# Kernel optimization log

Measured on AMD Instinct MI355X. Metric: run time of the kernel, lower is better.

## Reference

```python
import jax, jax.numpy as jnp
import numpy as np

EPS = 1e-5

def layernorm(x, g, b):
    xf = x.astype(jnp.float32)
    mu = jnp.mean(xf, axis=-1, keepdims=True)
    var = jnp.mean(jnp.square(xf - mu), axis=-1, keepdims=True)
    return ((xf - mu) * jax.lax.rsqrt(var + EPS) * g + b).astype(x.dtype)

def setup_inputs() -> dict:
    key = jax.random.key(0)
    ks = jax.random.split(key, 8)
    B, L, D_NODE, D_PAIR = 2, 512, 256, 128
    single = jax.random.normal(ks[0], (B, L, D_NODE), dtype=jnp.float32)
    pair = jax.random.normal(ks[1], (B, L, L, D_PAIR), dtype=jnp.float32)
    s = 1.0 / np.sqrt(D_NODE)
    Wa = jax.random.normal(ks[2], (D_PAIR, D_NODE), dtype=jnp.float32) * s
    ba = jnp.zeros((D_PAIR,), jnp.float32)
    Wb = jax.random.normal(ks[3], (D_PAIR, D_NODE), dtype=jnp.float32) * s
    bb = jnp.zeros((D_PAIR,), jnp.float32)
    # out layer is init='final' (zeros) in the original; use small random weights
    # so the reference output is non-trivial (same math).
    Wo = jax.random.normal(ks[4], (D_PAIR, D_PAIR), dtype=jnp.float32) * (1.0 / np.sqrt(D_PAIR))
    bo = jnp.zeros((D_PAIR,), jnp.float32)
    norm_g = jnp.ones((D_NODE,), jnp.float32)
    norm_b = jnp.zeros((D_NODE,), jnp.float32)
    pnorm_g = jnp.ones((D_PAIR,), jnp.float32)
    pnorm_b = jnp.zeros((D_PAIR,), jnp.float32)
    return dict(single=single, pair=pair, norm_g=norm_g, norm_b=norm_b,
                Wa=Wa, ba=ba, Wb=Wb, bb=bb, Wo=Wo, bo=bo,
                pnorm_g=pnorm_g, pnorm_b=pnorm_b)

def reference(single, pair, norm_g, norm_b, Wa, ba, Wb, bb, Wo, bo, pnorm_g, pnorm_b):
    x = layernorm(single, norm_g, norm_b)          # (B, L, D_NODE)
    a = x @ Wa.T + ba                               # (B, L, D_PAIR)
    b = x @ Wb.T + bb                               # (B, L, D_PAIR)
    outer = jnp.einsum('bid,bjd->bijd', a, b)       # (B, L, L, D_PAIR)
    upd = outer @ Wo.T + bo                         # (B, L, L, D_PAIR)
    return layernorm(pair + upd, pnorm_g, pnorm_b)
```

## Files before the change

### kernel.cpp

```cpp
#include <hip/hip_runtime.h>

#define BB   2
#define LL   512
#define DN   256
#define DP   128
#define TJ   64
#define LDSW 136

using bf16x8 = __attribute__((ext_vector_type(8))) short;
using f32x4  = __attribute__((ext_vector_type(4))) float;

__device__ inline unsigned short f2bf(float f) {
    unsigned int u = __float_as_uint(f);
    u += 0x7FFFu + ((u >> 16) & 1u);
    return (unsigned short)(u >> 16);
}

__global__ __launch_bounds__(256) void pu_ln_ab(
    const float* __restrict__ single, const float* __restrict__ norm_g,
    const float* __restrict__ norm_b, const float* __restrict__ Wa,
    const float* __restrict__ ba, const float* __restrict__ Wb,
    const float* __restrict__ bbias, float* __restrict__ abuf,
    unsigned short* __restrict__ bbuf)
{
    __shared__ __attribute__((aligned(16))) float xs[DN];
    __shared__ float red[8];
    const int row = blockIdx.x;
    const int tid = threadIdx.x;

    float v = single[row * DN + tid];
    float s1 = v, s2 = v * v;
    #pragma unroll
    for (int m = 32; m; m >>= 1) {
        s1 += __shfl_xor(s1, m);
        s2 += __shfl_xor(s2, m);
    }
    const int w = tid >> 6;
    if ((tid & 63) == 0) { red[w] = s1; red[4 + w] = s2; }
    __syncthreads();
    s1 = red[0] + red[1] + red[2] + red[3];
    s2 = red[4] + red[5] + red[6] + red[7];
    const float mu  = s1 * (1.0f / DN);
    const float var = s2 * (1.0f / DN) - mu * mu;
    const float rs  = rsqrtf(var + 1e-5f);
    xs[tid] = (v - mu) * rs * norm_g[tid] + norm_b[tid];
    __syncthreads();

    const int half = tid >> 7, p = tid & 127;
    const float4* W4 = (const float4*)((half ? Wb : Wa) + p * DN);
    const float4* x4 = (const float4*)xs;
    float acc = 0.f;
    #pragma unroll 8
    for (int d = 0; d < DN / 4; d++) {
        float4 wv = W4[d], xv = x4[d];
        acc += wv.x * xv.x + wv.y * xv.y + wv.z * xv.z + wv.w * xv.w;
    }
    acc += (half ? bbias[p] : ba[p]);
    if (half == 0) abuf[row * DP + p] = acc;
    else           bbuf[row * DP + p] = f2bf(acc);
}

__global__ __launch_bounds__(256) void pu_outer_ln(
    const float* __restrict__ pr, const float* __restrict__ Wo,
    const float* __restrict__ bo, const float* __restrict__ png,
    const float* __restrict__ pnb, const float* __restrict__ abuf,
    const unsigned short* __restrict__ bbuf, float* __restrict__ out)
{
    __shared__ __attribute__((aligned(16))) unsigned short sW[DP * LDSW];
    __shared__ __attribute__((aligned(16))) unsigned short sB[TJ * LDSW];

    const int jt  = blockIdx.x;
    const int i   = blockIdx.y;
    const int bz  = blockIdx.z;
    const int tid = threadIdx.x;
    const int j0  = jt * TJ;

    const int lane = tid & 63;
    const int w    = tid >> 6;
    const int m    = lane & 15;
    const int q    = lane >> 4;

    const size_t obase = (((size_t)bz * LL + i) * LL + (j0 + w * 16)) * DP;
    float pv[4][8];
    #pragma unroll
    for (int r = 0; r < 4; r++) {
        const size_t rowoff = obase + (size_t)(q * 4 + r) * DP + m;
        #pragma unroll
        for (int t = 0; t < 8; t++) pv[r][t] = pr[rowoff + t * 16];
    }

    float bo_r[8], g_r[8], pb_r[8];
    #pragma unroll
    for (int t = 0; t < 8; t++) {
        bo_r[t] = bo[t * 16 + m];
        g_r[t]  = png[t * 16 + m];
        pb_r[t] = pnb[t * 16 + m];
    }

    const float* arow = abuf + ((size_t)bz * LL + i) * DP;
    #pragma unroll
    for (int e = 0; e < 8; e++) {
        const int v  = tid + e * 256;
        const int pw = v >> 4;
        const int d0 = (v & 15) * 8;
        const float4* w4 = (const float4*)(Wo + pw * DP + d0);
        const float4* a4 = (const float4*)(arow + d0);
        float4 wa = w4[0], wb = w4[1], aa = a4[0], ab = a4[1];
        uint4 pk;
        pk.x = (unsigned)f2bf(wa.x * aa.x) | ((unsigned)f2bf(wa.y * aa.y) << 16);
        pk.y = (unsigned)f2bf(wa.z * aa.z) | ((unsigned)f2bf(wa.w * aa.w) << 16);
        pk.z = (unsigned)f2bf(wb.x * ab.x) | ((unsigned)f2bf(wb.y * ab.y) << 16);
        pk.w = (unsigned)f2bf(wb.z * ab.z) | ((unsigned)f2bf(wb.w * ab.w) << 16);
        *(uint4*)&sW[pw * LDSW + d0] = pk;
    }

    const uint4* bsrc = (const uint4*)(bbuf + ((size_t)bz * LL + j0) * DP);
    #pragma unroll
    for (int e = 0; e < 4; e++) {
        const int v  = tid + e * 256;
        const int jr = v >> 4;
        const int d0 = (v & 15) * 8;
        *(uint4*)&sB[jr * LDSW + d0] = bsrc[v];
    }
    __syncthreads();

    f32x4 acc[8];
    #pragma unroll
    for (int t = 0; t < 8; t++) { f32x4 z = {0.f, 0.f, 0.f, 0.f}; acc[t] = z; }

    const unsigned short* Abase = sB + (w * 16 + m) * LDSW + q * 8;
    const unsigned short* Bbase = sW + m * LDSW + q * 8;
    #pragma unroll
    for (int s = 0; s < 4; s++) {
        bf16x8 af = *(const bf16x8*)(Abase + s * 32);
        #pragma unroll
        for (int t = 0; t < 8; t++) {
            bf16x8 bf = *(const bf16x8*)(Bbase + t * 16 * LDSW + s * 32);
            acc[t] = __builtin_amdgcn_mfma_f32_16x16x32_bf16(af, bf, acc[t], 0, 0, 0);
        }
    }

    #pragma unroll
    for (int r = 0; r < 4; r++) {
        const size_t rowoff = obase + (size_t)(q * 4 + r) * DP + m;
        float v[8], s1 = 0.f, s2 = 0.f;
        #pragma unroll
        for (int t = 0; t < 8; t++) {
            v[t] = pv[r][t] + acc[t][r] + bo_r[t];
            s1 += v[t];
            s2 += v[t] * v[t];
        }
        s1 += __shfl_xor(s1, 1); s2 += __shfl_xor(s2, 1);
        s1 += __shfl_xor(s1, 2); s2 += __shfl_xor(s2, 2);
        s1 += __shfl_xor(s1, 4); s2 += __shfl_xor(s2, 4);
        s1 += __shfl_xor(s1, 8); s2 += __shfl_xor(s2, 8);
        const float mu  = s1 * (1.0f / DP);
        const float var = s2 * (1.0f / DP) - mu * mu;
        const float rs  = rsqrtf(var + 1e-5f);
        #pragma unroll
        for (int t = 0; t < 8; t++)
            out[rowoff + t * 16] = (v[t] - mu) * rs * g_r[t] + pb_r[t];
    }
}

extern "C" void kernel_launch(void* const* d_in, const int* in_sizes, int n_in,
                              void* d_out, int out_size, void* d_ws, size_t ws_size,
                              hipStream_t stream) {
    const float* single = (const float*)d_in[0];
    const float* pair   = (const float*)d_in[1];
    const float* norm_g = (const float*)d_in[2];
    const float* norm_b = (const float*)d_in[3];
    const float* Wa     = (const float*)d_in[4];
    const float* ba     = (const float*)d_in[5];
    const float* Wb     = (const float*)d_in[6];
    const float* bb     = (const float*)d_in[7];
    const float* Wo     = (const float*)d_in[8];
    const float* bo     = (const float*)d_in[9];
    const float* png    = (const float*)d_in[10];
    const float* pnb    = (const float*)d_in[11];
    float* out = (float*)d_out;

    float* abuf = (float*)d_ws;
    unsigned short* bbuf =
        (unsigned short*)((char*)d_ws + (size_t)BB * LL * DP * sizeof(float));

    pu_ln_ab<<<dim3(BB * LL), dim3(256), 0, stream>>>(
        single, norm_g, norm_b, Wa, ba, Wb, bb, abuf, bbuf);

    pu_outer_ln<<<dim3(LL / TJ, LL, BB), dim3(256), 0, stream>>>(
        pair, Wo, bo, png, pnb, abuf, bbuf, out);
}
```

Measured before the change: 529.3 us.

## Loop over all j-tiles per block to reuse scaled Wo tile across chunks

```diff
diff --git a/kernel.cpp b/kernel.cpp
--- a/kernel.cpp
+++ b/kernel.cpp
@@ -60,41 +60,45 @@
     else           bbuf[row * DP + p] = f2bf(acc);
 }
 
-__global__ __launch_bounds__(256) void pu_outer_ln(
+__global__ __launch_bounds__(256, 4) void pu_outer_ln(
     const float* __restrict__ pr, const float* __restrict__ Wo,
     const float* __restrict__ bo, const float* __restrict__ png,
     const float* __restrict__ pnb, const float* __restrict__ abuf,
     const unsigned short* __restrict__ bbuf, float* __restrict__ out)
 {
     __shared__ __attribute__((aligned(16))) unsigned short sW[DP * LDSW];
-    __shared__ __attribute__((aligned(16))) unsigned short sB[TJ * LDSW];
-
-    const int jt  = blockIdx.x;
-    const int i   = blockIdx.y;
-    const int bz  = blockIdx.z;
-    const int tid = threadIdx.x;
-    const int j0  = jt * TJ;
-
+
+    const int i    = blockIdx.x;
+    const int bz   = blockIdx.y;
+    const int tid  = threadIdx.x;
     const int lane = tid & 63;
     const int w    = tid >> 6;
     const int m    = lane & 15;
     const int q    = lane >> 4;
 
-    const size_t obase = (((size_t)bz * LL + i) * LL + (j0 + w * 16)) * DP;
-    float pv[4][8];
-    #pragma unroll
-    for (int r = 0; r < 4; r++) {
-        const size_t rowoff = obase + (size_t)(q * 4 + r) * DP + m;
-        #pragma unroll
-        for (int t = 0; t < 8; t++) pv[r][t] = pr[rowoff + t * 16];
-    }
-
     float bo_r[8], g_r[8], pb_r[8];
     #pragma unroll
     for (int t = 0; t < 8; t++) {
         bo_r[t] = bo[t * 16 + m];
         g_r[t]  = png[t * 16 + m];
         pb_r[t] = pnb[t * 16 + m];
+    }
+
+    const size_t ibase = (((size_t)bz * LL + i) * LL) * DP;
+    const unsigned short* bbb = bbuf + (size_t)bz * LL * DP;
+
+    float pv[4][8];
+    #pragma unroll
+    for (int r = 0; r < 4; r++) {
+        const size_t rowoff = ibase + (size_t)(w * 16 + q * 4 + r) * DP + m;
+        #pragma unroll
+        for (int t = 0; t < 8; t++) pv[r][t] = pr[rowoff + t * 16];
+    }
+    bf16x8 afr[4];
+    {
+        const unsigned short* brow = bbb + (size_t)(w * 16 + m) * DP + q * 8;
+        #pragma unroll
+        for (int s = 0; s < 4; s++) afr[s] = *(const bf16x8*)(brow + s * 32);
     }
 
     const float* arow = abuf + ((size_t)bz * LL + i) * DP;
@@ -113,53 +117,66 @@
         pk.w = (unsigned)f2bf(wb.z * ab.z) | ((unsigned)f2bf(wb.w * ab.w) << 16);
         *(uint4*)&sW[pw * LDSW + d0] = pk;
     }
-
-    const uint4* bsrc = (const uint4*)(bbuf + ((size_t)bz * LL + j0) * DP);
-    #pragma unroll
-    for (int e = 0; e < 4; e++) {
-        const int v  = tid + e * 256;
-        const int jr = v >> 4;
-        const int d0 = (v & 15) * 8;
-        *(uint4*)&sB[jr * LDSW + d0] = bsrc[v];
-    }
     __syncthreads();
 
-    f32x4 acc[8];
-    #pragma unroll
-    for (int t = 0; t < 8; t++) { f32x4 z = {0.f, 0.f, 0.f, 0.f}; acc[t] = z; }
-
-    const unsigned short* Abase = sB + (w * 16 + m) * LDSW + q * 8;
     const unsigned short* Bbase = sW + m * LDSW + q * 8;
-    #pragma unroll
-    for (int s = 0; s < 4; s++) {
-        bf16x8 af = *(const bf16x8*)(Abase + s * 32);
-        #pragma unroll
-        for (int t = 0; t < 8; t++) {
-            bf16x8 bf = *(const bf16x8*)(Bbase + t * 16 * LDSW + s * 32);
-            acc[t] = __builtin_amdgcn_mfma_f32_16x16x32_bf16(af, bf, acc[t], 0, 0, 0);
-        }
-    }
-
-    #pragma unroll
-    for (int r = 0; r < 4; r++) {
-        const size_t rowoff = obase + (size_t)(q * 4 + r) * DP + m;
-        float v[8], s1 = 0.f, s2 = 0.f;
-        #pragma unroll
-        for (int t = 0; t < 8; t++) {
-            v[t] = pv[r][t] + acc[t][r] + bo_r[t];
-            s1 += v[t];
-            s2 += v[t] * v[t];
-        }
-        s1 += __shfl_xor(s1, 1); s2 += __shfl_xor(s2, 1);
-        s1 += __shfl_xor(s1, 2); s2 += __shfl_xor(s2, 2);
-        s1 += __shfl_xor(s1, 4); s2 += __shfl_xor(s2, 4);
-        s1 += __shfl_xor(s1, 8); s2 += __shfl_xor(s2, 8);
-        const float mu  = s1 * (1.0f / DP);
-        const float var = s2 * (1.0f / DP) - mu * mu;
-        const float rs  = rsqrtf(var + 1e-5f);
-        #pragma unroll
-        for (int t = 0; t < 8; t++)
-            out[rowoff + t * 16] = (v[t] - mu) * rs * g_r[t] + pb_r[t];
+
+    for (int jc = 0; jc < 8; jc++) {
+        const int j0 = jc * TJ;
+
+        f32x4 acc[8];
+        #pragma unroll
+        for (int t = 0; t < 8; t++) { f32x4 z = {0.f, 0.f, 0.f, 0.f}; acc[t] = z; }
+
+        #pragma unroll
+        for (int s = 0; s < 4; s++) {
+            bf16x8 af = afr[s];
+            #pragma unroll
+            for (int t = 0; t < 8; t++) {
+                bf16x8 bfv = *(const bf16x8*)(Bbase + t * 16 * LDSW + s * 32);
+                acc[t] = __builtin_amdgcn_mfma_f32_16x16x32_bf16(af, bfv, acc[t], 0, 0, 0);
+            }
+        }
+
+        if (jc < 7) {
+            const unsigned short* brow =
+                bbb + (size_t)(j0 + TJ + w * 16 + m) * DP + q * 8;
+            #pragma unroll
+            for (int s = 0; s < 4; s++) afr[s] = *(const bf16x8*)(brow + s * 32);
+        }
+
+        const size_t obase = ibase + (size_t)(j0 + w * 16) * DP;
+        #pragma unroll
+        for (int r = 0; r < 4; r++) {
+            const size_t rowoff = obase + (size_t)(q * 4 + r) * DP + m;
+            float v[8], s1 = 0.f, s2 = 0.f;
+            #pragma unroll
+            for (int t = 0; t < 8; t++) {
+                v[t] = pv[r][t] + acc[t][r] + bo_r[t];
+                s1 += v[t];
+                s2 += v[t] * v[t];
+            }
+            s1 += __shfl_xor(s1, 1); s2 += __shfl_xor(s2, 1);
+            s1 += __shfl_xor(s1, 2); s2 += __shfl_xor(s2, 2);
+            s1 += __shfl_xor(s1, 4); s2 += __shfl_xor(s2, 4);
+            s1 += __shfl_xor(s1, 8); s2 += __shfl_xor(s2, 8);
+            const float mu  = s1 * (1.0f / DP);
+            const float var = s2 * (1.0f / DP) - mu * mu;
+            const float rs  = rsqrtf(var + 1e-5f);
+            #pragma unroll
+            for (int t = 0; t < 8; t++)
+                out[rowoff + t * 16] = (v[t] - mu) * rs * g_r[t] + pb_r[t];
+        }
+
+        if (jc < 7) {
+            const size_t nb = ibase + (size_t)(j0 + TJ + w * 16) * DP;
+            #pragma unroll
+            for (int r = 0; r < 4; r++) {
+                const size_t rowoff = nb + (size_t)(q * 4 + r) * DP + m;
+                #pragma unroll
+                for (int t = 0; t < 8; t++) pv[r][t] = pr[rowoff + t * 16];
+            }
+        }
     }
 }
 
@@ -187,6 +204,6 @@
     pu_ln_ab<<<dim3(BB * LL), dim3(256), 0, stream>>>(
         single, norm_g, norm_b, Wa, ba, Wb, bb, abuf, bbuf);
 
-    pu_outer_ln<<<dim3(LL / TJ, LL, BB), dim3(256), 0, stream>>>(
+    pu_outer_ln<<<dim3(LL, BB), dim3(256), 0, stream>>>(
         pair, Wo, bo, png, pnb, abuf, bbuf, out);
 }
```

Measured after the change: 645.5 us. +22.0%, slower.
